# Performance work log

Measured on AMD Instinct MI355X. Metric: run time of the kernel, lower is better.

## Reference

```python
import jax, jax.numpy as jnp
import numpy as np
import math

B, QL, KL, D, H, FF = 2, 2048, 2048, 512, 8, 2048
DH = D // H

def layernorm(x, g, b, eps=1e-5):
    m = jnp.mean(x, axis=-1, keepdims=True)
    v = jnp.mean((x - m) ** 2, axis=-1, keepdims=True)
    return (x - m) * jax.lax.rsqrt(v + eps) * g + b

def mha(x, mask, wq, bq, wk, bk, wv, bv, wo, bo, kv=None):
    # faithful port of MultiHeadAttention.forward (eval mode, dropout off)
    bs, qlen, dim = x.shape
    src = x if kv is None else kv
    def split(t):
        return t.reshape(bs, -1, H, DH).transpose(0, 2, 1, 3)  # [b,h,l,dh]
    q = split(x @ wq + bq) * (1.0 / math.sqrt(DH))
    k = split(src @ wk + bk)
    v = split(src @ wv + bv)
    scores = jnp.einsum('bhqd,bhkd->bhqk', q, k)
    m = mask[:, None, :, :] if mask.ndim == 3 else mask[:, None, None, :]
    scores = jnp.where(m == 0, -jnp.inf, scores)
    w = jax.nn.softmax(scores.astype(jnp.float32), axis=-1).astype(scores.dtype)
    ctx = jnp.einsum('bhqk,bhkd->bhqd', w, v)
    ctx = ctx.transpose(0, 2, 1, 3).reshape(bs, qlen, dim)
    return ctx @ wo + bo

def decoder_layer(tgt, memory, pos, tkpm, causal_mask, mem_mask,
                  sa, ca, l1w, l1b, l2w, l2b, n1g, n1b, n2g, n2b, n3g, n3b):
    tgt = tgt + pos
    t2 = layernorm(tgt, n1g, n1b)
    t2 = t2 * tkpm[:, :, None]
    t2 = mha(t2, causal_mask, *sa)
    tgt = tgt + t2
    t2 = layernorm(tgt, n2g, n2b)
    t2 = mha(t2, mem_mask, *ca, kv=memory)
    tgt = tgt + t2
    t2 = layernorm(tgt, n3g, n3b)
    t2 = jax.nn.relu(t2 @ l1w + l1b) @ l2w + l2b
    tgt = tgt + t2
    tgt = tgt * tkpm[:, :, None]
    return tgt

def setup_inputs() -> dict:
    key = jax.random.key(0)
    ks = jax.random.split(key, 32)
    it = iter(list(ks))
    def nrm(shape, s=0.02):
        return jax.random.normal(next(it), shape, jnp.float32) * s
    inp = {}
    inp['cfg'] = 0
    inp['tgt'] = jax.random.normal(next(it), (B, QL, D), jnp.float32)
    inp['memory'] = jax.random.normal(next(it), (B, KL, D), jnp.float32)
    inp['pos'] = jax.random.normal(next(it), (B, QL, D), jnp.float32)
    inp['causal_mask'] = jnp.broadcast_to(jnp.tril(jnp.ones((QL, QL), jnp.int32)), (B, QL, QL))
    inp['tgt_key_padding_mask'] = jnp.ones((B, QL), jnp.float32)
    mkpm = jax.random.randint(next(it), (B, KL), 0, 2).astype(jnp.int32)
    inp['memory_key_padding_mask'] = mkpm.at[:, 0].set(1)  # avoid fully-masked rows
    for p in ['sa', 'ca']:
        for w in ['q', 'k', 'v', 'o']:
            inp[f'{p}_{w}_w'] = nrm((D, D))
            inp[f'{p}_{w}_b'] = jnp.zeros((D,), jnp.float32)
    inp['lin1_w'] = nrm((D, FF)); inp['lin1_b'] = jnp.zeros((FF,), jnp.float32)
    inp['lin2_w'] = nrm((FF, D)); inp['lin2_b'] = jnp.zeros((D,), jnp.float32)
    for n in ['n1', 'n2', 'n3']:
        inp[f'{n}_g'] = jnp.ones((D,), jnp.float32)
        inp[f'{n}_b'] = jnp.zeros((D,), jnp.float32)
    return inp

def reference(cfg, tgt, memory, pos, causal_mask, tgt_key_padding_mask, memory_key_padding_mask,
              sa_q_w, sa_q_b, sa_k_w, sa_k_b, sa_v_w, sa_v_b, sa_o_w, sa_o_b,
              ca_q_w, ca_q_b, ca_k_w, ca_k_b, ca_v_w, ca_v_b, ca_o_w, ca_o_b,
              lin1_w, lin1_b, lin2_w, lin2_b,
              n1_g, n1_b, n2_g, n2_b, n3_g, n3_b):
    sa = (sa_q_w, sa_q_b, sa_k_w, sa_k_b, sa_v_w, sa_v_b, sa_o_w, sa_o_b)
    ca = (ca_q_w, ca_q_b, ca_k_w, ca_k_b, ca_v_w, ca_v_b, ca_o_w, ca_o_b)
    return decoder_layer(tgt, memory, pos, tgt_key_padding_mask, causal_mask, memory_key_padding_mask,
                         sa, ca, lin1_w, lin1_b, lin2_w, lin2_b, n1_g, n1_b, n2_g, n2_b, n3_g, n3_b)
```

## Files before the change

kernel.cpp:

```cpp
#include <hip/hip_runtime.h>
#include <hip/hip_bf16.h>
#include <stdint.h>

#define QL   2048
#define KLn  2048
#define DIM  512
#define NH   8
#define DH   64
#define NB   2
#define MROWS (NB*QL)
#define FFD  2048

typedef unsigned short u16;
typedef unsigned int u32;
typedef __attribute__((ext_vector_type(8))) short short8;
typedef __attribute__((ext_vector_type(4))) float f32x4;

__device__ __forceinline__ u16 f2b(float f){
  union { float f; u32 i; } v; v.f = f;
  u32 r = v.i + 0x7FFFu + ((v.i >> 16) & 1u);
  return (u16)(r >> 16);
}
__device__ __forceinline__ float b2f(u16 u){
  union { u32 i; float f; } v; v.i = ((u32)u) << 16; return v.f;
}
__device__ __forceinline__ u32 cvtpk(float a, float b){
  u32 r;
  asm("v_cvt_pk_bf16_f32 %0, %1, %2" : "=v"(r) : "v"(a), "v"(b));
  return r;
}

typedef __attribute__((address_space(3))) void as3void;
typedef __attribute__((address_space(1))) void as1void;
__device__ __forceinline__ void gload_lds16(const void* g, void* l){
  __builtin_amdgcn_global_load_lds((as1void*)g, (as3void*)l, 16, 0, 0);
}

#define BK 64
enum { EPI_BIAS=0, EPI_SCALEQ=1, EPI_RELU=2, EPI_RES=3, EPI_FIN=5, EPI_QKV=6, EPI_KV=7 };
#define QSCALE 0.1803368801111244f

template<int EPI>
__global__ __launch_bounds__(256, 4)
void gemm64(const u16* __restrict__ A, const u16* __restrict__ Bt,
            const float* __restrict__ bias,
            u16* __restrict__ Obf, float* __restrict__ Ores,
            const float* __restrict__ tk, float* __restrict__ fout,
            int K, int N)
{
  __shared__ __align__(16) u16 As[64*BK];
  __shared__ __align__(16) u16 Bs[64*BK];
  const int t  = threadIdx.x;
  const int l  = t & 63;
  const int lq = l & 15, lg = l >> 4;
  const int w  = t >> 6;
  const int wm = (w >> 1) * 32;
  const int wn = (w & 1) * 32;

  const int gx   = gridDim.x;
  const int nwg  = gx * gridDim.y;
  const int orig = blockIdx.x + gx * blockIdx.y;
  const int wgid = (orig & 7) * (nwg >> 3) + (orig >> 3);
  const int m0 = (wgid / gx) * 64;
  const int n0 = (wgid % gx) * 64;

  const int srow = t >> 3;
  const int scs  = t & 7;

  auto stage = [&](int k0){
    #pragma unroll
    for (int i = 0; i < 2; ++i){
      const int row = i*32 + srow;
      gload_lds16(A  + (size_t)(m0 + row)*K + k0 + ((scs ^ (row & 7)) << 3),
                  &As[row*BK + scs*8]);
      gload_lds16(Bt + (size_t)(n0 + row)*K + k0 + ((scs ^ (row & 7)) << 3),
                  &Bs[row*BK + scs*8]);
    }
  };

  f32x4 acc[2][2];
  #pragma unroll
  for (int i=0;i<2;i++)
    #pragma unroll
    for (int j=0;j<2;j++) acc[i][j] = (f32x4){0.f,0.f,0.f,0.f};

  stage(0);
  for (int k0 = 0; k0 < K; k0 += BK){
    __syncthreads();
    short8 af[2][2], bf[2][2];
    #pragma unroll
    for (int kc = 0; kc < 2; ++kc){
      #pragma unroll
      for (int i=0;i<2;i++){
        af[i][kc] = *(const short8*)&As[(wm + i*16 + lq)*BK + (((kc*4 + lg) ^ (lq & 7)) << 3)];
        bf[i][kc] = *(const short8*)&Bs[(wn + i*16 + lq)*BK + (((kc*4 + lg) ^ (lq & 7)) << 3)];
      }
    }
    __syncthreads();
    if (k0 + BK < K) stage(k0 + BK);
    __builtin_amdgcn_s_setprio(1);
    #pragma unroll
    for (int kc = 0; kc < 2; ++kc)
      #pragma unroll
      for (int i=0;i<2;i++)
        #pragma unroll
        for (int j=0;j<2;j++)
          acc[i][j] = __builtin_amdgcn_mfma_f32_16x16x32_bf16(af[i][kc], bf[j][kc], acc[i][j], 0,0,0);
    __builtin_amdgcn_s_setprio(0);
  }

  #pragma unroll
  for (int i=0;i<2;i++){
    #pragma unroll
    for (int j=0;j<2;j++){
      #pragma unroll
      for (int rr=0;rr<4;rr++){
        const int row = m0 + wm + i*16 + lg*4 + rr;
        const int col = n0 + wn + j*16 + lq;
        float v = acc[i][j][rr] + bias[col];
        if (EPI == EPI_SCALEQ) v *= QSCALE;
        if (EPI == EPI_RELU)   v = fmaxf(v, 0.f);
        if (EPI == EPI_RES)    Ores[(size_t)row*N + col] += v;
        else if (EPI == EPI_FIN){
          const size_t idx = (size_t)row*N + col;
          fout[idx] = (Ores[idx] + v) * tk[row];
        }
        else if (EPI == EPI_QKV){
          const int seg = col >> 9, c = col & 511;
          if (seg == 0)      Obf[(size_t)row*512 + c] = f2b(v * QSCALE);
          else if (seg == 1){
            const int bb = row >> 11, kv = row & 2047;
            const int hh = c >> 6,  dh = c & 63;
            Obf[(2u<<20) + ((((size_t)(bb*NH + hh) << 11) + kv) << 6) + (dh ^ ((kv & 7) << 3))] = f2b(v);
          }
          else               Obf[(4u<<20) + (size_t)row*512 + c] = f2b(v);
        }
        else if (EPI == EPI_KV){
          const int seg = col >> 9, c = col & 511;
          if (seg == 0){
            const int bb = row >> 11, kv = row & 2047;
            const int hh = c >> 6,  dh = c & 63;
            Obf[((((size_t)(bb*NH + hh) << 11) + kv) << 6) + (dh ^ ((kv & 7) << 3))] = f2b(v);
          }
          else               Obf[(2u<<20) + (size_t)row*512 + c] = f2b(v);
        }
        else                   Obf[(size_t)row*N + col] = f2b(v);
      }
    }
  }
}

template<bool CAUSAL>
__global__ __launch_bounds__(256, 4)
void attn6(const u16* __restrict__ Q, const u16* __restrict__ Kbh,
           const u16* __restrict__ Vth, const float* __restrict__ bias,
           u16* __restrict__ ctxp, float2* __restrict__ mlb)
{
  __shared__ __align__(16) u16 Kl[2][64*64];
  __shared__ __align__(16) u16 Vl[2][64*64];
  const int tid = threadIdx.x;
  const int l  = tid & 63;
  const int w  = tid >> 6;
  const int lq = l & 15, lg = l >> 4;
  const int h    = blockIdx.y;
  const int b    = blockIdx.z >> 1;
  const int half = blockIdx.z & 1;
  const int qtile = CAUSAL ? ((b & 1) ? (31 - (int)blockIdx.x) : (int)blockIdx.x)
                           : (int)blockIdx.x;
  const int q0w = qtile*64 + w*16;

  const u16* kg = Kbh + ((size_t)(b*NH + h) << 17);
  const u16* vg = Vth + ((size_t)(b*NH + h) << 17);

  short8 aq[2];
  #pragma unroll
  for (int kc = 0; kc < 2; ++kc)
    aq[kc] = *(const short8*)(Q + (size_t)(b*QL + q0w + lq)*DIM + h*DH + kc*32 + lg*8);

  f32x4 ctx[4];
  #pragma unroll
  for (int d = 0; d < 4; ++d) ctx[d] = (f32x4){0.f,0.f,0.f,0.f};
  f32x4 lsum4 = (f32x4){0.f,0.f,0.f,0.f};
  float m = -INFINITY;

  const int ntiles = CAUSAL ? (qtile + 1) : (KLn >> 6);

  auto stage = [&](int buf, int t){
    const int kvs = t*64;
    #pragma unroll
    for (int i = 0; i < 2; ++i){
      gload_lds16(kg + (size_t)kvs*64 + w*1024 + i*512 + l*8,
                  &Kl[buf][w*1024 + i*512 + l*8]);
      gload_lds16(vg + (size_t)(w*16 + i*8 + (l>>3))*KLn + kvs + (l&7)*8,
                  &Vl[buf][w*1024 + i*512 + l*8]);
    }
  };

  stage(0, half);
  __syncthreads();
  int cur = 0;

  for (int t = half; t < ntiles; t += 2){
    if (t + 2 < ntiles) stage(cur ^ 1, t + 2);
    const int kvs = t*64;
    f32x4 s[4];
    #pragma unroll
    for (int sub = 0; sub < 4; ++sub) s[sub] = (f32x4){0.f,0.f,0.f,0.f};
    __builtin_amdgcn_s_setprio(1);
    #pragma unroll
    for (int sub = 0; sub < 4; ++sub){
      const int r = sub*16 + lq;
      #pragma unroll
      for (int kc = 0; kc < 2; ++kc){
        short8 bk = *(const short8*)&Kl[cur][r*64 + (((kc*4 + lg) ^ (r & 7)) << 3)];
        s[sub] = __builtin_amdgcn_mfma_f32_16x16x32_bf16(bk, aq[kc], s[sub], 0,0,0);
      }
    }
    __builtin_amdgcn_s_setprio(0);
    if (CAUSAL){
      if (kvs + 63 > q0w){
        #pragma unroll
        for (int sub = 0; sub < 4; ++sub)
          #pragma unroll
          for (int rr = 0; rr < 4; ++rr)
            if (kvs + sub*16 + lg*4 + rr > q0w + lq) s[sub][rr] = -INFINITY;
      }
    } else {
      #pragma unroll
      for (int sub = 0; sub < 4; ++sub){
        f32x4 bv = *(const f32x4*)(bias + b*KLn + kvs + sub*16 + lg*4);
        s[sub] += bv;
      }
    }
    float mx[4];
    #pragma unroll
    for (int sub = 0; sub < 4; ++sub)
      mx[sub] = fmaxf(fmaxf(s[sub][0], s[sub][1]), fmaxf(s[sub][2], s[sub][3]));
    float pmax = fmaxf(fmaxf(mx[0], mx[1]), fmaxf(mx[2], mx[3]));
    if (!__all(pmax <= m + 8.0f)){
      pmax = fmaxf(pmax, __shfl_xor(pmax, 16));
      pmax = fmaxf(pmax, __shfl_xor(pmax, 32));
      const float mnew = fmaxf(m, pmax);
      const float corr = exp2f(m - mnew);
      lsum4 *= corr;
      float corr4[4];
      #pragma unroll
      for (int rr = 0; rr < 4; ++rr) corr4[rr] = __shfl(corr, lg*4 + rr);
      #pragma unroll
      for (int d = 0; d < 4; ++d)
        #pragma unroll
        for (int rr = 0; rr < 4; ++rr) ctx[d][rr] *= corr4[rr];
      m = mnew;
    }
    u32 pk[4][2];
    #pragma unroll
    for (int sub = 0; sub < 4; ++sub){
      float p0 = exp2f(s[sub][0] - m);
      float p1 = exp2f(s[sub][1] - m);
      float p2 = exp2f(s[sub][2] - m);
      float p3 = exp2f(s[sub][3] - m);
      lsum4 += (f32x4){p0, p1, p2, p3};
      pk[sub][0] = cvtpk(p0, p1);
      pk[sub][1] = cvtpk(p2, p3);
    }
    union { u32 u[4]; short8 s8; } pa0, pa1;
    pa0.u[0] = pk[0][0]; pa0.u[1] = pk[0][1]; pa0.u[2] = pk[1][0]; pa0.u[3] = pk[1][1];
    pa1.u[0] = pk[2][0]; pa1.u[1] = pk[2][1]; pa1.u[2] = pk[3][0]; pa1.u[3] = pk[3][1];
    __builtin_amdgcn_s_setprio(1);
    #pragma unroll
    for (int d0 = 0; d0 < 4; ++d0){
      const int dl = d0*16 + lq;
      short8 v0 = *(const short8*)&Vl[cur][dl*64 + ((lg       ^ (dl & 7)) << 3)];
      short8 v1 = *(const short8*)&Vl[cur][dl*64 + (((4 + lg) ^ (dl & 7)) << 3)];
      ctx[d0] = __builtin_amdgcn_mfma_f32_16x16x32_bf16(pa0.s8, v0, ctx[d0], 0,0,0);
      ctx[d0] = __builtin_amdgcn_mfma_f32_16x16x32_bf16(pa1.s8, v1, ctx[d0], 0,0,0);
    }
    __builtin_amdgcn_s_setprio(0);
    __syncthreads();
    cur ^= 1;
  }

  float hs = (lsum4[0] + lsum4[1]) + (lsum4[2] + lsum4[3]);
  hs += __shfl_xor(hs, 16);
  hs += __shfl_xor(hs, 32);
  if (lg == 0)
    mlb[((size_t)((half*NB + b)*NH + h) << 11) + q0w + lq] = make_float2(m, hs);
  u16* cp = ctxp + (size_t)half*MROWS*DIM;
  #pragma unroll
  for (int d0 = 0; d0 < 4; ++d0)
    #pragma unroll
    for (int rr = 0; rr < 4; ++rr)
      cp[(size_t)(b*QL + q0w + lg*4 + rr)*DIM + h*DH + d0*16 + lq] = f2b(ctx[d0][rr]);
}

__global__ __launch_bounds__(256)
void attn_merge(const u16* __restrict__ ctxp, const float2* __restrict__ mlb,
                u16* __restrict__ O)
{
  const int idx = blockIdx.x*256 + threadIdx.x;
  const int row = idx >> 7;
  const int col = (idx & 127) * 4;
  const int b = row >> 11, qr = row & 2047, h = col >> 6;
  const float2 a0 = mlb[((size_t)((      b)*NH + h) << 11) + qr];
  const float2 a1 = mlb[((size_t)((NB  + b)*NH + h) << 11) + qr];
  const float mg = fmaxf(a0.x, a1.x);
  const float w0 = exp2f(a0.x - mg), w1 = exp2f(a1.x - mg);
  const float rden = 1.f / (a0.y*w0 + a1.y*w1);
  union { uint2 v; u16 h4[4]; } c0u, c1u;
  c0u.v = *(const uint2*)&ctxp[(size_t)row*DIM + col];
  c1u.v = *(const uint2*)&ctxp[(size_t)MROWS*DIM + (size_t)row*DIM + col];
  u16 o[4];
  #pragma unroll
  for (int i = 0; i < 4; ++i)
    o[i] = f2b((b2f(c0u.h4[i])*w0 + b2f(c1u.h4[i])*w1) * rden);
  *(uint2*)&O[(size_t)row*DIM + col] = *(const uint2*)o;
}

template<int MODE>
__global__ __launch_bounds__(128)
void ln_kernel(const float* __restrict__ in0, const float* __restrict__ in1,
               const float* __restrict__ tkpm,
               const float* __restrict__ g, const float* __restrict__ bvec,
               float* __restrict__ xres, u16* __restrict__ outb)
{
  const int row = blockIdx.x;
  const int t = threadIdx.x;
  float v[4];
  #pragma unroll
  for (int i = 0; i < 4; ++i){
    const int c = t + i*128;
    float x = in0[(size_t)row*DIM + c];
    if (MODE == 0){
      x += in1[(size_t)row*DIM + c];
      xres[(size_t)row*DIM + c] = x;
    }
    v[i] = x;
  }
  float s = v[0]+v[1]+v[2]+v[3];
  #pragma unroll
  for (int off = 1; off < 64; off <<= 1) s += __shfl_xor(s, off);
  __shared__ float red[4];
  if ((t & 63) == 0) red[t >> 6] = s;
  __syncthreads();
  const float mean = (red[0] + red[1]) * (1.f/512.f);
  float q = 0.f;
  #pragma unroll
  for (int i = 0; i < 4; ++i){ const float d = v[i]-mean; q += d*d; }
  #pragma unroll
  for (int off = 1; off < 64; off <<= 1) q += __shfl_xor(q, off);
  if ((t & 63) == 0) red[2 + (t >> 6)] = q;
  __syncthreads();
  const float var = (red[2] + red[3]) * (1.f/512.f);
  const float rs = rsqrtf(var + 1e-5f);
  const float tk = (MODE == 0) ? tkpm[row] : 1.f;
  #pragma unroll
  for (int i = 0; i < 4; ++i){
    const int c = t + i*128;
    const float y = (v[i] - mean) * rs * g[c] + bvec[c];
    outb[(size_t)row*DIM + c] = f2b(y * tk);
  }
}

__global__ __launch_bounds__(256)
void prep_all(const float* w0, const float* w1, const float* w2, const float* w3,
              const float* w4, const float* w5, const float* w6, const float* w7,
              const float* __restrict__ mem, const int* __restrict__ mkpm,
              const float* saqb, const float* sakb, const float* savb,
              const float* cakb, const float* cavb,
              u16* __restrict__ wtA, u16* __restrict__ memb,
              float* __restrict__ bias, float* __restrict__ bc0,
              float* __restrict__ bc1)
{
  __shared__ float tile[32][33];
  const int id = blockIdx.x;
  const int tid = threadIdx.x;
  if (id < 2048){
    const int z = id >> 8, rem = id & 255;
    const int r0 = (rem >> 4) * 32, c0 = (rem & 15) * 32;
    const float* wp[8] = {w0,w1,w2,w3,w4,w5,w6,w7};
    const float* w = wp[z];
    u16* o = wtA + (size_t)z * 512 * 512;
    const int tx = tid & 31, ty = tid >> 5;
    #pragma unroll
    for (int i = 0; i < 4; ++i)
      tile[ty + i*8][tx] = w[(size_t)(r0 + ty + i*8)*512 + c0 + tx];
    __syncthreads();
    #pragma unroll
    for (int i = 0; i < 4; ++i)
      o[(size_t)(c0 + ty + i*8)*512 + r0 + tx] = f2b(tile[tx][ty + i*8]);
  } else if (id < 4096){
    const int i = (id - 2048)*1024 + tid*4;
    f32x4 v = *(const f32x4*)&mem[i];
    uint2 p; p.x = cvtpk(v[0], v[1]); p.y = cvtpk(v[2], v[3]);
    *(uint2*)&memb[i] = p;
  } else {
    const int j = (id - 4096)*256 + tid;
    bias[j] = mkpm[j] ? 0.f : -1e30f;
    if (j < 1536) bc0[j] = (j < 512) ? saqb[j] : (j < 1024) ? sakb[j-512] : savb[j-1024];
    if (j < 1024) bc1[j] = (j < 512) ? cakb[j] : cavb[j-512];
  }
}

__global__ __launch_bounds__(256)
void transpose_vperm(const u16* __restrict__ in, u16* __restrict__ out)
{
  __shared__ u16 tile[32][33];
  in  += (size_t)blockIdx.z * KLn * DIM;
  out += (size_t)blockIdx.z * NH * DH * KLn;
  const int tx = threadIdx.x, ty = threadIdx.y;
  const int r0 = blockIdx.y*32, c0 = blockIdx.x*32;
  #pragma unroll
  for (int i = 0; i < 4; ++i)
    tile[ty + i*8][tx] = in[(size_t)(r0 + ty + i*8)*DIM + c0 + tx];
  __syncthreads();
  const int kv = r0 + tx;
  const int s  = (kv & ~31) | (((kv>>2)&3)<<3) | (((kv>>4)&1)<<2) | (kv&3);
  #pragma unroll
  for (int i = 0; i < 4; ++i){
    const int dcol = c0 + ty + i*8;
    const int hh = dcol >> 6, dh = dcol & 63;
    const int kvpos = (s & ~63) | (((((s>>3)&7) ^ (dh&7)) << 3)) | (s & 7);
    out[((size_t)(hh*DH + dh))*KLn + kvpos] = tile[tx][ty + i*8];
  }
}

__global__ __launch_bounds__(256)
void prep_cross(const u16* __restrict__ vb, u16* __restrict__ vt,
                const float* __restrict__ l1w, u16* __restrict__ l1wt,
                const float* __restrict__ l2w, u16* __restrict__ l2wt)
{
  const int id = blockIdx.x;
  const int tid = threadIdx.x;
  const int tx = tid & 31, ty = tid >> 5;
  if (id < 2048){
    __shared__ u16 tileu[32][33];
    const int z = id >> 10, rem = id & 1023;
    const int c0 = (rem & 15) * 32, r0 = (rem >> 4) * 32;
    const u16* in = vb + (size_t)z * KLn * DIM;
    u16* out = vt + (size_t)z * NH * DH * KLn;
    #pragma unroll
    for (int i = 0; i < 4; ++i)
      tileu[ty + i*8][tx] = in[(size_t)(r0 + ty + i*8)*DIM + c0 + tx];
    __syncthreads();
    const int kv = r0 + tx;
    const int s  = (kv & ~31) | (((kv>>2)&3)<<3) | (((kv>>4)&1)<<2) | (kv&3);
    #pragma unroll
    for (int i = 0; i < 4; ++i){
      const int dcol = c0 + ty + i*8;
      const int hh = dcol >> 6, dh = dcol & 63;
      const int kvpos = (s & ~63) | (((((s>>3)&7) ^ (dh&7)) << 3)) | (s & 7);
      out[((size_t)(hh*DH + dh))*KLn + kvpos] = tileu[tx][ty + i*8];
    }
  } else {
    __shared__ float tilef[32][33];
    const float* in; u16* out; int R, C, rem;
    if (id < 3072){ rem = id - 2048; in = l1w; out = l1wt; R = 512; C = FFD;
      const int c0 = (rem & 63) * 32, r0 = (rem >> 6) * 32;
      #pragma unroll
      for (int i = 0; i < 4; ++i)
        tilef[ty + i*8][tx] = in[(size_t)(r0 + ty + i*8)*C + c0 + tx];
      __syncthreads();
      #pragma unroll
      for (int i = 0; i < 4; ++i)
        out[(size_t)(c0 + ty + i*8)*R + r0 + tx] = f2b(tilef[tx][ty + i*8]);
    } else { rem = id - 3072; in = l2w; out = l2wt; R = FFD; C = 512;
      const int c0 = (rem & 15) * 32, r0 = (rem >> 4) * 32;
      #pragma unroll
      for (int i = 0; i < 4; ++i)
        tilef[ty + i*8][tx] = in[(size_t)(r0 + ty + i*8)*C + c0 + tx];
      __syncthreads();
      #pragma unroll
      for (int i = 0; i < 4; ++i)
        out[(size_t)(c0 + ty + i*8)*R + r0 + tx] = f2b(tilef[tx][ty + i*8]);
    }
  }
}

extern "C" void kernel_launch(void* const* d_in, const int* in_sizes, int n_in,
                              void* d_out, int out_size, void* d_ws, size_t ws_size,
                              hipStream_t stream)
{
  const float* tgt  = (const float*)d_in[1];
  const float* mem  = (const float*)d_in[2];
  const float* pos  = (const float*)d_in[3];
  const float* tkpm = (const float*)d_in[5];
  const int*   mkpm = (const int*)d_in[6];
  const float* saqw = (const float*)d_in[7];  const float* saqb = (const float*)d_in[8];
  const float* sakw = (const float*)d_in[9];  const float* sakb = (const float*)d_in[10];
  const float* savw = (const float*)d_in[11]; const float* savb = (const float*)d_in[12];
  const float* saow = (const float*)d_in[13]; const float* saob = (const float*)d_in[14];
  const float* caqw = (const float*)d_in[15]; const float* caqb = (const float*)d_in[16];
  const float* cakw = (const float*)d_in[17]; const float* cakb = (const float*)d_in[18];
  const float* cavw = (const float*)d_in[19]; const float* cavb = (const float*)d_in[20];
  const float* caow = (const float*)d_in[21]; const float* caob = (const float*)d_in[22];
  const float* l1w  = (const float*)d_in[23]; const float* l1b  = (const float*)d_in[24];
  const float* l2w  = (const float*)d_in[25]; const float* l2b  = (const float*)d_in[26];
  const float* n1g  = (const float*)d_in[27]; const float* n1b  = (const float*)d_in[28];
  const float* n2g  = (const float*)d_in[29]; const float* n2b  = (const float*)d_in[30];
  const float* n3g  = (const float*)d_in[31]; const float* n3b  = (const float*)d_in[32];

  if (ws_size < 58720256) return;

  char* ws = (char*)d_ws;
  float* xres = (float*)(ws);
  u16* t2n    = (u16*)(ws + (8u<<20));
  u16* qb     = (u16*)(ws + (12u<<20));
  u16* kb     = (u16*)(ws + (16u<<20));
  u16* vb     = (u16*)(ws + (20u<<20));
  u16* vt     = (u16*)(ws + (24u<<20));
  float* bias = (float*)(ws + (28u<<20));
  float* bc0  = (float*)(ws + (28u<<20) + 16384);
  float* bc1  = (float*)(ws + (28u<<20) + 24576);
  float2* mlb = (float2*)(ws + (28u<<20) + 32768);
  u16* l1wt   = (u16*)(ws + (29u<<20));
  u16* l2wt   = (u16*)(ws + (31u<<20));
  u16* memb   = (u16*)(ws + (33u<<20));
  u16* wtA    = (u16*)(ws + (37u<<20));
  u16* ctxp   = (u16*)(ws + (41u<<20));
  u16* ffh    = (u16*)(ws + (12u<<20));

  float* out = (float*)d_out;
  const int W55 = 512*512;

  prep_all<<<dim3(4112), 256, 0, stream>>>(saqw, sakw, savw, saow,
                                           caqw, cakw, cavw, caow,
                                           mem, mkpm, saqb, sakb, savb, cakb, cavb,
                                           wtA, memb, bias, bc0, bc1);
  ln_kernel<0><<<MROWS, 128, 0, stream>>>(tgt, pos, tkpm, n1g, n1b, xres, t2n);

  #define G(EP, GX) gemm64<EP><<<dim3(GX,64), 256, 0, stream>>>

  G(EPI_QKV, 24)(t2n, wtA, bc0, qb, nullptr, nullptr, nullptr, 512, 1536);
  transpose_vperm<<<dim3(DIM/32, KLn/32, NB), dim3(32,8), 0, stream>>>(vb, vt);
  attn6<true><<<dim3(QL/64, NH, NB*2), 256, 0, stream>>>(qb, kb, vt, nullptr, ctxp, mlb);
  attn_merge<<<dim3(MROWS*DIM/1024), 256, 0, stream>>>(ctxp, mlb, t2n);
  G(EPI_RES, 8)(t2n, wtA + 3*W55, saob, nullptr, xres, nullptr, nullptr, 512, 512);

  ln_kernel<1><<<MROWS, 128, 0, stream>>>(xres, nullptr, nullptr, n2g, n2b, nullptr, t2n);

  G(EPI_SCALEQ, 8)(t2n,  wtA + 4*W55, caqb, qb, nullptr, nullptr, nullptr, 512, 512);
  G(EPI_KV, 16)(memb, wtA + 5*W55, bc1, kb, nullptr, nullptr, nullptr, 512, 1024);
  prep_cross<<<dim3(4096), 256, 0, stream>>>(vb, vt, l1w, l1wt, l2w, l2wt);
  attn6<false><<<dim3(QL/64, NH, NB*2), 256, 0, stream>>>(qb, kb, vt, bias, ctxp, mlb);
  attn_merge<<<dim3(MROWS*DIM/1024), 256, 0, stream>>>(ctxp, mlb, t2n);
  G(EPI_RES, 8)(t2n, wtA + 7*W55, caob, nullptr, xres, nullptr, nullptr, 512, 512);

  ln_kernel<1><<<MROWS, 128, 0, stream>>>(xres, nullptr, nullptr, n3g, n3b, nullptr, t2n);

  G(EPI_RELU, 32)(t2n, l1wt, l1b, ffh, nullptr, nullptr, nullptr, 512, FFD);
  G(EPI_FIN, 8)(ffh, l2wt, l2b, nullptr, xres, tkpm, out, 2048, 512);

  #undef G
}
```

Baseline: 194.0 us.

## Double-buffer GEMM LDS and use explicit vmcnt waits in attention pipeline

```diff
diff --git a/kernel.cpp b/kernel.cpp
--- a/kernel.cpp
+++ b/kernel.cpp
@@ -48,8 +48,8 @@
             const float* __restrict__ tk, float* __restrict__ fout,
             int K, int N)
 {
-  __shared__ __align__(16) u16 As[64*BK];
-  __shared__ __align__(16) u16 Bs[64*BK];
+  __shared__ __align__(16) u16 As[2][64*BK];
+  __shared__ __align__(16) u16 Bs[2][64*BK];
   const int t  = threadIdx.x;
   const int l  = t & 63;
   const int lq = l & 15, lg = l >> 4;
@@ -67,53 +67,72 @@
   const int srow = t >> 3;
   const int scs  = t & 7;
 
-  auto stage = [&](int k0){
-    #pragma unroll
+  auto stageG = [&](u16* dA, u16* dB, int k0){
+    _Pragma("unroll")
     for (int i = 0; i < 2; ++i){
       const int row = i*32 + srow;
       gload_lds16(A  + (size_t)(m0 + row)*K + k0 + ((scs ^ (row & 7)) << 3),
-                  &As[row*BK + scs*8]);
+                  dA + row*BK + scs*8);
       gload_lds16(Bt + (size_t)(n0 + row)*K + k0 + ((scs ^ (row & 7)) << 3),
-                  &Bs[row*BK + scs*8]);
+                  dB + row*BK + scs*8);
     }
   };
 
+  int aoff[2][2], boff[2][2];
+  _Pragma("unroll")
+  for (int i = 0; i < 2; ++i)
+    _Pragma("unroll")
+    for (int kc = 0; kc < 2; ++kc){
+      const int sw = (((kc*4 + lg) ^ (lq & 7)) << 3);
+      aoff[i][kc] = ((wm + i*16 + lq)*BK + sw) * 2;
+      boff[i][kc] = ((wn + i*16 + lq)*BK + sw) * 2;
+    }
+
   f32x4 acc[2][2];
-  #pragma unroll
+  _Pragma("unroll")
   for (int i=0;i<2;i++)
-    #pragma unroll
+    _Pragma("unroll")
     for (int j=0;j<2;j++) acc[i][j] = (f32x4){0.f,0.f,0.f,0.f};
 
-  stage(0);
-  for (int k0 = 0; k0 < K; k0 += BK){
-    __syncthreads();
-    short8 af[2][2], bf[2][2];
-    #pragma unroll
-    for (int kc = 0; kc < 2; ++kc){
-      #pragma unroll
-      for (int i=0;i<2;i++){
-        af[i][kc] = *(const short8*)&As[(wm + i*16 + lq)*BK + (((kc*4 + lg) ^ (lq & 7)) << 3)];
-        bf[i][kc] = *(const short8*)&Bs[(wn + i*16 + lq)*BK + (((kc*4 + lg) ^ (lq & 7)) << 3)];
-      }
-    }
-    __syncthreads();
-    if (k0 + BK < K) stage(k0 + BK);
-    __builtin_amdgcn_s_setprio(1);
-    #pragma unroll
-    for (int kc = 0; kc < 2; ++kc)
-      #pragma unroll
-      for (int i=0;i<2;i++)
-        #pragma unroll
-        for (int j=0;j<2;j++)
-          acc[i][j] = __builtin_amdgcn_mfma_f32_16x16x32_bf16(af[i][kc], bf[j][kc], acc[i][j], 0,0,0);
-    __builtin_amdgcn_s_setprio(0);
-  }
-
-  #pragma unroll
+#define GBODY(BUF, KK)                                                        \
+  {                                                                           \
+    { const int ks = ((KK) + BK < K) ? (KK) + BK : 0;                         \
+      stageG(As[(BUF)^1], Bs[(BUF)^1], ks); }                                 \
+    asm volatile("s_waitcnt vmcnt(4)" ::: "memory");                          \
+    __builtin_amdgcn_s_barrier();                                             \
+    __builtin_amdgcn_sched_barrier(0);                                        \
+    short8 af[2][2], bf[2][2];                                                \
+    _Pragma("unroll")                                                         \
+    for (int kc = 0; kc < 2; ++kc)                                            \
+      _Pragma("unroll")                                                       \
+      for (int i = 0; i < 2; ++i){                                            \
+        af[i][kc] = *(const short8*)((const char*)As + (BUF)*8192 + aoff[i][kc]); \
+        bf[i][kc] = *(const short8*)((const char*)Bs + (BUF)*8192 + boff[i][kc]); \
+      }                                                                       \
+    __builtin_amdgcn_s_barrier();                                             \
+    __builtin_amdgcn_s_setprio(1);                                            \
+    _Pragma("unroll")                                                         \
+    for (int kc = 0; kc < 2; ++kc)                                            \
+      _Pragma("unroll")                                                       \
+      for (int i = 0; i < 2; ++i)                                             \
+        _Pragma("unroll")                                                     \
+        for (int j = 0; j < 2; ++j)                                           \
+          acc[i][j] = __builtin_amdgcn_mfma_f32_16x16x32_bf16(af[i][kc], bf[j][kc], acc[i][j], 0,0,0); \
+    __builtin_amdgcn_s_setprio(0);                                            \
+  }
+
+  stageG(As[0], Bs[0], 0);
+  for (int k0 = 0; k0 < K; k0 += 2*BK){
+    GBODY(0, k0)
+    GBODY(1, k0 + BK)
+  }
+#undef GBODY
+
+  _Pragma("unroll")
   for (int i=0;i<2;i++){
-    #pragma unroll
+    _Pragma("unroll")
     for (int j=0;j<2;j++){
-      #pragma unroll
+      _Pragma("unroll")
       for (int rr=0;rr<4;rr++){
         const int row = m0 + wm + i*16 + lg*4 + rr;
         const int col = n0 + wn + j*16 + lq;
@@ -152,7 +171,7 @@
 
 template<bool CAUSAL>
 __global__ __launch_bounds__(256, 4)
-void attn6(const u16* __restrict__ Q, const u16* __restrict__ Kbh,
+void attn7(const u16* __restrict__ Q, const u16* __restrict__ Kbh,
            const u16* __restrict__ Vth, const float* __restrict__ bias,
            u16* __restrict__ ctxp, float2* __restrict__ mlb)
 {
@@ -173,112 +192,132 @@
   const u16* vg = Vth + ((size_t)(b*NH + h) << 17);
 
   short8 aq[2];
-  #pragma unroll
+  _Pragma("unroll")
   for (int kc = 0; kc < 2; ++kc)
     aq[kc] = *(const short8*)(Q + (size_t)(b*QL + q0w + lq)*DIM + h*DH + kc*32 + lg*8);
 
+  int koff[4][2], voff[4][2];
+  _Pragma("unroll")
+  for (int j = 0; j < 4; ++j)
+    _Pragma("unroll")
+    for (int kc = 0; kc < 2; ++kc){
+      const int sw = (((kc*4 + lg) ^ (lq & 7)) << 3);
+      koff[j][kc] = ((j*16 + lq)*64 + sw) * 2;
+      voff[j][kc] = koff[j][kc];
+    }
+
   f32x4 ctx[4];
-  #pragma unroll
+  _Pragma("unroll")
   for (int d = 0; d < 4; ++d) ctx[d] = (f32x4){0.f,0.f,0.f,0.f};
   f32x4 lsum4 = (f32x4){0.f,0.f,0.f,0.f};
   float m = -INFINITY;
 
   const int ntiles = CAUSAL ? (qtile + 1) : (KLn >> 6);
-
-  auto stage = [&](int buf, int t){
-    const int kvs = t*64;
-    #pragma unroll
-    for (int i = 0; i < 2; ++i){
-      gload_lds16(kg + (size_t)kvs*64 + w*1024 + i*512 + l*8,
-                  &Kl[buf][w*1024 + i*512 + l*8]);
-      gload_lds16(vg + (size_t)(w*16 + i*8 + (l>>3))*KLn + kvs + (l&7)*8,
-                  &Vl[buf][w*1024 + i*512 + l*8]);
-    }
+  const int P = (ntiles > half) ? ((ntiles - half + 1) >> 1) : 0;
+
+  auto stageA = [&](u16* dK, u16* dV, int tile){
+    const u16* kgs = kg + ((size_t)tile << 12);
+    const u16* vgs = vg + tile*64;
+    gload_lds16(kgs + w*1024 + l*8,       dK + w*1024 + l*8);
+    gload_lds16(kgs + w*1024 + 512 + l*8, dK + w*1024 + 512 + l*8);
+    gload_lds16(vgs + (size_t)(w*16 +     (l>>3))*KLn + (l&7)*8, dV + w*1024 + l*8);
+    gload_lds16(vgs + (size_t)(w*16 + 8 + (l>>3))*KLn + (l&7)*8, dV + w*1024 + 512 + l*8);
   };
 
-  stage(0, half);
-  __syncthreads();
-  int cur = 0;
-
-  for (int t = half; t < ntiles; t += 2){
-    if (t + 2 < ntiles) stage(cur ^ 1, t + 2);
-    const int kvs = t*64;
-    f32x4 s[4];
-    #pragma unroll
-    for (int sub = 0; sub < 4; ++sub) s[sub] = (f32x4){0.f,0.f,0.f,0.f};
-    __builtin_amdgcn_s_setprio(1);
-    #pragma unroll
-    for (int sub = 0; sub < 4; ++sub){
-      const int r = sub*16 + lq;
-      #pragma unroll
-      for (int kc = 0; kc < 2; ++kc){
-        short8 bk = *(const short8*)&Kl[cur][r*64 + (((kc*4 + lg) ^ (r & 7)) << 3)];
-        s[sub] = __builtin_amdgcn_mfma_f32_16x16x32_bf16(bk, aq[kc], s[sub], 0,0,0);
-      }
-    }
-    __builtin_amdgcn_s_setprio(0);
-    if (CAUSAL){
-      if (kvs + 63 > q0w){
-        #pragma unroll
-        for (int sub = 0; sub < 4; ++sub)
-          #pragma unroll
-          for (int rr = 0; rr < 4; ++rr)
-            if (kvs + sub*16 + lg*4 + rr > q0w + lq) s[sub][rr] = -INFINITY;
-      }
-    } else {
-      #pragma unroll
-      for (int sub = 0; sub < 4; ++sub){
-        f32x4 bv = *(const f32x4*)(bias + b*KLn + kvs + sub*16 + lg*4);
-        s[sub] += bv;
-      }
-    }
-    float mx[4];
-    #pragma unroll
-    for (int sub = 0; sub < 4; ++sub)
-      mx[sub] = fmaxf(fmaxf(s[sub][0], s[sub][1]), fmaxf(s[sub][2], s[sub][3]));
-    float pmax = fmaxf(fmaxf(mx[0], mx[1]), fmaxf(mx[2], mx[3]));
-    if (!__all(pmax <= m + 8.0f)){
-      pmax = fmaxf(pmax, __shfl_xor(pmax, 16));
-      pmax = fmaxf(pmax, __shfl_xor(pmax, 32));
-      const float mnew = fmaxf(m, pmax);
-      const float corr = exp2f(m - mnew);
-      lsum4 *= corr;
-      float corr4[4];
-      #pragma unroll
-      for (int rr = 0; rr < 4; ++rr) corr4[rr] = __shfl(corr, lg*4 + rr);
-      #pragma unroll
-      for (int d = 0; d < 4; ++d)
-        #pragma unroll
-        for (int rr = 0; rr < 4; ++rr) ctx[d][rr] *= corr4[rr];
-      m = mnew;
-    }
-    u32 pk[4][2];
-    #pragma unroll
-    for (int sub = 0; sub < 4; ++sub){
-      float p0 = exp2f(s[sub][0] - m);
-      float p1 = exp2f(s[sub][1] - m);
-      float p2 = exp2f(s[sub][2] - m);
-      float p3 = exp2f(s[sub][3] - m);
-      lsum4 += (f32x4){p0, p1, p2, p3};
-      pk[sub][0] = cvtpk(p0, p1);
-      pk[sub][1] = cvtpk(p2, p3);
-    }
-    union { u32 u[4]; short8 s8; } pa0, pa1;
-    pa0.u[0] = pk[0][0]; pa0.u[1] = pk[0][1]; pa0.u[2] = pk[1][0]; pa0.u[3] = pk[1][1];
-    pa1.u[0] = pk[2][0]; pa1.u[1] = pk[2][1]; pa1.u[2] = pk[3][0]; pa1.u[3] = pk[3][1];
-    __builtin_amdgcn_s_setprio(1);
-    #pragma unroll
-    for (int d0 = 0; d0 < 4; ++d0){
-      const int dl = d0*16 + lq;
-      short8 v0 = *(const short8*)&Vl[cur][dl*64 + ((lg       ^ (dl & 7)) << 3)];
-      short8 v1 = *(const short8*)&Vl[cur][dl*64 + (((4 + lg) ^ (dl & 7)) << 3)];
-      ctx[d0] = __builtin_amdgcn_mfma_f32_16x16x32_bf16(pa0.s8, v0, ctx[d0], 0,0,0);
-      ctx[d0] = __builtin_amdgcn_mfma_f32_16x16x32_bf16(pa1.s8, v1, ctx[d0], 0,0,0);
-    }
-    __builtin_amdgcn_s_setprio(0);
-    __syncthreads();
-    cur ^= 1;
-  }
+#define ABODY(BUF, TT)                                                        \
+  {                                                                           \
+    f32x4 bv[4];                                                              \
+    if (!CAUSAL){                                                             \
+      _Pragma("unroll")                                                       \
+      for (int sub = 0; sub < 4; ++sub)                                       \
+        bv[sub] = *(const f32x4*)(bias + b*KLn + (TT)*64 + sub*16 + lg*4);    \
+    }                                                                         \
+    { const int ts = ((TT) + 2 < ntiles) ? (TT) + 2 : half;                   \
+      stageA(Kl[(BUF)^1], Vl[(BUF)^1], ts); }                                 \
+    if (CAUSAL) asm volatile("s_waitcnt vmcnt(4)" ::: "memory");              \
+    else        asm volatile("s_waitcnt vmcnt(8)" ::: "memory");              \
+    __builtin_amdgcn_s_barrier();                                             \
+    __builtin_amdgcn_sched_barrier(0);                                        \
+    f32x4 s[4];                                                               \
+    _Pragma("unroll")                                                         \
+    for (int sub = 0; sub < 4; ++sub) s[sub] = (f32x4){0.f,0.f,0.f,0.f};      \
+    __builtin_amdgcn_s_setprio(1);                                            \
+    _Pragma("unroll")                                                         \
+    for (int sub = 0; sub < 4; ++sub)                                         \
+      _Pragma("unroll")                                                       \
+      for (int kc = 0; kc < 2; ++kc){                                         \
+        short8 bk = *(const short8*)((const char*)Kl + (BUF)*8192 + koff[sub][kc]); \
+        s[sub] = __builtin_amdgcn_mfma_f32_16x16x32_bf16(bk, aq[kc], s[sub], 0,0,0); \
+      }                                                                       \
+    __builtin_amdgcn_s_setprio(0);                                            \
+    if (CAUSAL){                                                              \
+      if ((TT)*64 + 63 > q0w){                                                \
+        _Pragma("unroll")                                                     \
+        for (int sub = 0; sub < 4; ++sub)                                     \
+          _Pragma("unroll")                                                   \
+          for (int rr = 0; rr < 4; ++rr)                                      \
+            if ((TT)*64 + sub*16 + lg*4 + rr > q0w + lq) s[sub][rr] = -INFINITY; \
+      }                                                                       \
+    } else {                                                                  \
+      _Pragma("unroll")                                                       \
+      for (int sub = 0; sub < 4; ++sub) s[sub] += bv[sub];                    \
+    }                                                                         \
+    float mx[4];                                                              \
+    _Pragma("unroll")                                                         \
+    for (int sub = 0; sub < 4; ++sub)                                         \
+      mx[sub] = fmaxf(fmaxf(s[sub][0], s[sub][1]), fmaxf(s[sub][2], s[sub][3])); \
+    float pmax = fmaxf(fmaxf(mx[0], mx[1]), fmaxf(mx[2], mx[3]));             \
+    if (!__all(pmax <= m + 8.0f)){                                            \
+      pmax = fmaxf(pmax, __shfl_xor(pmax, 16));                               \
+      pmax = fmaxf(pmax, __shfl_xor(pmax, 32));                               \
+      const float mnew = fmaxf(m, pmax);                                      \
+      const float corr = exp2f(m - mnew);                                     \
+      lsum4 *= corr;                                                          \
+      float corr4[4];                                                         \
+      _Pragma("unroll")                                                       \
+      for (int rr = 0; rr < 4; ++rr) corr4[rr] = __shfl(corr, lg*4 + rr);     \
+      _Pragma("unroll")                                                       \
+      for (int d = 0; d < 4; ++d)                                             \
+        _Pragma("unroll")                                                     \
+        for (int rr = 0; rr < 4; ++rr) ctx[d][rr] *= corr4[rr];               \
+      m = mnew;                                                               \
+    }                                                                         \
+    u32 pk[4][2];                                                             \
+    _Pragma("unroll")                                                         \
+    for (int sub = 0; sub < 4; ++sub){                                        \
+      float p0 = exp2f(s[sub][0] - m);                                        \
+      float p1 = exp2f(s[sub][1] - m);                                        \
+      float p2 = exp2f(s[sub][2] - m);                                        \
+      float p3 = exp2f(s[sub][3] - m);                                        \
+      lsum4 += (f32x4){p0, p1, p2, p3};                                       \
+      pk[sub][0] = cvtpk(p0, p1);                                             \
+      pk[sub][1] = cvtpk(p2, p3);                                             \
+    }                                                                         \
+    union { u32 u[4]; short8 s8; } pa0, pa1;                                  \
+    pa0.u[0] = pk[0][0]; pa0.u[1] = pk[0][1]; pa0.u[2] = pk[1][0]; pa0.u[3] = pk[1][1]; \
+    pa1.u[0] = pk[2][0]; pa1.u[1] = pk[2][1]; pa1.u[2] = pk[3][0]; pa1.u[3] = pk[3][1]; \
+    __builtin_amdgcn_s_setprio(1);                                            \
+    _Pragma("unroll")                                                         \
+    for (int d0 = 0; d0 < 4; ++d0){                                           \
+      short8 v0 = *(const short8*)((const char*)Vl + (BUF)*8192 + voff[d0][0]); \
+      short8 v1 = *(const short8*)((const char*)Vl + (BUF)*8192 + voff[d0][1]); \
+      ctx[d0] = __builtin_amdgcn_mfma_f32_16x16x32_bf16(pa0.s8, v0, ctx[d0], 0,0,0); \
+      ctx[d0] = __builtin_amdgcn_mfma_f32_16x16x32_bf16(pa1.s8, v1, ctx[d0], 0,0,0); \
+    }                                                                         \
+    __builtin_amdgcn_s_setprio(0);                                            \
+    __builtin_amdgcn_s_barrier();                                             \
+  }
+
+  if (P > 0){
+    stageA(Kl[0], Vl[0], half);
+    int t = half;
+    for (int it = 0; it < P; it += 2){
+      ABODY(0, t)
+      if (it + 1 < P) ABODY(1, t + 2)
+      t += 4;
+    }
+  }
+#undef ABODY
 
   float hs = (lsum4[0] + lsum4[1]) + (lsum4[2] + lsum4[3]);
   hs += __shfl_xor(hs, 16);
@@ -286,9 +325,9 @@
   if (lg == 0)
     mlb[((size_t)((half*NB + b)*NH + h) << 11) + q0w + lq] = make_float2(m, hs);
   u16* cp = ctxp + (size_t)half*MROWS*DIM;
-  #pragma unroll
+  _Pragma("unroll")
   for (int d0 = 0; d0 < 4; ++d0)
-    #pragma unroll
+    _Pragma("unroll")
     for (int rr = 0; rr < 4; ++rr)
       cp[(size_t)(b*QL + q0w + lg*4 + rr)*DIM + h*DH + d0*16 + lq] = f2b(ctx[d0][rr]);
 }
@@ -453,25 +492,26 @@
     }
   } else {
     __shared__ float tilef[32][33];
-    const float* in; u16* out; int R, C, rem;
-    if (id < 3072){ rem = id - 2048; in = l1w; out = l1wt; R = 512; C = FFD;
+    if (id < 3072){
+      const int rem = id - 2048;
       const int c0 = (rem & 63) * 32, r0 = (rem >> 6) * 32;
       #pragma unroll
       for (int i = 0; i < 4; ++i)
-        tilef[ty + i*8][tx] = in[(size_t)(r0 + ty + i*8)*C + c0 + tx];
+        tilef[ty + i*8][tx] = l1w[(size_t)(r0 + ty + i*8)*FFD + c0 + tx];
       __syncthreads();
       #pragma unroll
       for (int i = 0; i < 4; ++i)
-        out[(size_t)(c0 + ty + i*8)*R + r0 + tx] = f2b(tilef[tx][ty + i*8]);
-    } else { rem = id - 3072; in = l2w; out = l2wt; R = FFD; C = 512;
+        l1wt[(size_t)(c0 + ty + i*8)*512 + r0 + tx] = f2b(tilef[tx][ty + i*8]);
+    } else {
+      const int rem = id - 3072;
       const int c0 = (rem & 15) * 32, r0 = (rem >> 4) * 32;
       #pragma unroll
       for (int i = 0; i < 4; ++i)
-        tilef[ty + i*8][tx] = in[(size_t)(r0 + ty + i*8)*C + c0 + tx];
+        tilef[ty + i*8][tx] = l2w[(size_t)(r0 + ty + i*8)*512 + c0 + tx];
       __syncthreads();
       #pragma unroll
       for (int i = 0; i < 4; ++i)
-        out[(size_t)(c0 + ty + i*8)*R + r0 + tx] = f2b(tilef[tx][ty + i*8]);
+        l2wt[(size_t)(c0 + ty + i*8)*FFD + r0 + tx] = f2b(tilef[tx][ty + i*8]);
     }
   }
 }
@@ -532,7 +572,7 @@
 
   G(EPI_QKV, 24)(t2n, wtA, bc0, qb, nullptr, nullptr, nullptr, 512, 1536);
   transpose_vperm<<<dim3(DIM/32, KLn/32, NB), dim3(32,8), 0, stream>>>(vb, vt);
-  attn6<true><<<dim3(QL/64, NH, NB*2), 256, 0, stream>>>(qb, kb, vt, nullptr, ctxp, mlb);
+  attn7<true><<<dim3(QL/64, NH, NB*2), 256, 0, stream>>>(qb, kb, vt, nullptr, ctxp, mlb);
   attn_merge<<<dim3(MROWS*DIM/1024), 256, 0, stream>>>(ctxp, mlb, t2n);
   G(EPI_RES, 8)(t2n, wtA + 3*W55, saob, nullptr, xres, nullptr, nullptr, 512, 512);
 
@@ -541,7 +581,7 @@
   G(EPI_SCALEQ, 8)(t2n,  wtA + 4*W55, caqb, qb, nullptr, nullptr, nullptr, 512, 512);
   G(EPI_KV, 16)(memb, wtA + 5*W55, bc1, kb, nullptr, nullptr, nullptr, 512, 1024);
   prep_cross<<<dim3(4096), 256, 0, stream>>>(vb, vt, l1w, l1wt, l2w, l2wt);
-  attn6<false><<<dim3(QL/64, NH, NB*2), 256, 0, stream>>>(qb, kb, vt, bias, ctxp, mlb);
+  attn7<false><<<dim3(QL/64, NH, NB*2), 256, 0, stream>>>(qb, kb, vt, bias, ctxp, mlb);
   attn_merge<<<dim3(MROWS*DIM/1024), 256, 0, stream>>>(ctxp, mlb, t2n);
   G(EPI_RES, 8)(t2n, wtA + 7*W55, caob, nullptr, xres, nullptr, nullptr, 512, 512);
 
```

Result: no change. 193.2 us (-0.4%).
